# Kernel tuning notes

Hardware: AMD Instinct MI355X
Metric: run time of the kernel (lower is better)

The kernel has to match this reference:

```python
import jax, jax.numpy as jnp
import numpy as np

NUM_FREQ = 10
HIDDEN = 256
ENC_DIM = 2 * 2 * NUM_FREQ  # input_dim * 2 * num_frequencies = 40
OUT_DIM = 3


def setup_inputs() -> dict:
    key = jax.random.key(0)
    ks = jax.random.split(key, 8)
    B, N = 4, 262144
    x = jax.random.uniform(ks[0], (B, N, 2), dtype=jnp.float32)
    # layer 0: enc_dim -> hidden
    W_in = jax.random.normal(ks[1], (ENC_DIM, HIDDEN), dtype=jnp.float32) * (1.0 / np.sqrt(ENC_DIM))
    b_in = jnp.zeros((HIDDEN,), dtype=jnp.float32)
    # layers 1..6: hidden -> hidden (6 of them)
    W_hid = jax.random.normal(ks[2], (6, HIDDEN, HIDDEN), dtype=jnp.float32) * (1.0 / np.sqrt(HIDDEN))
    b_hid = jnp.zeros((6, HIDDEN), dtype=jnp.float32)
    # layer 7: hidden -> out
    W_out = jax.random.normal(ks[3], (HIDDEN, OUT_DIM), dtype=jnp.float32) * (1.0 / np.sqrt(HIDDEN))
    b_out = jnp.zeros((OUT_DIM,), dtype=jnp.float32)
    return {"x": x, "W_in": W_in, "b_in": b_in, "W_hid": W_hid,
            "b_hid": b_hid, "W_out": W_out, "b_out": b_out}


def _pos_encode(x):
    # x: (B, N, 2) -> (B, N, 40). Matches torch: cat([sin, cos], -1) over freq axis then flatten.
    freq = 2.0 ** jnp.arange(NUM_FREQ, dtype=jnp.float32)  # (10,)
    xe = x[..., :, None] * freq  # (B, N, 2, 10)
    enc = jnp.concatenate([jnp.sin(xe), jnp.cos(xe)], axis=-1)  # (B, N, 2, 20)
    return enc.reshape(x.shape[0], x.shape[1], -1)  # (B, N, 40)


def reference(x, W_in, b_in, W_hid, b_hid, W_out, b_out):
    h = _pos_encode(x)
    h = jax.nn.relu(h @ W_in + b_in)
    for i in range(W_hid.shape[0]):  # 6 hidden layers, fixed small loop
        h = jax.nn.relu(h @ W_hid[i] + b_hid[i])
    out = jnp.tanh(h @ W_out + b_out) / 100.0
    return out
```

## Files before the change

kernel.cpp:

```cpp
#include <hip/hip_runtime.h>
#include <stdint.h>

#define THREADS 256
#define NBLOCKS 8192
#define BR      128

#define NG_STRIDE 204800
#define WS_WOUT   819200
#define WS_TOTAL  (WS_WOUT + 16384)

typedef short bf16x8 __attribute__((ext_vector_type(8)));
typedef short bf16x4 __attribute__((ext_vector_type(4)));
typedef float f32x16 __attribute__((ext_vector_type(16)));
typedef float f32x4v __attribute__((ext_vector_type(4)));

__device__ __forceinline__ unsigned short f2bf(float f) {
    union { float f; unsigned int u; } v; v.f = f;
    unsigned int u = v.u;
    u += 0x7fffu + ((u >> 16) & 1u);
    return (unsigned short)(u >> 16);
}
__device__ __forceinline__ unsigned int cvt_pk_bf16(float lo, float hi) {
    unsigned int d;
    asm("v_cvt_pk_bf16_f32 %0, %1, %2" : "=v"(d) : "v"(lo), "v"(hi));
    return d;
}
__device__ __forceinline__ bf16x8 ld_act(const unsigned char* lo,
                                         const unsigned char* hi) {
    bf16x4 a = *(const bf16x4*)lo;
    bf16x4 b = *(const bf16x4*)hi;
    return __builtin_shufflevector(a, b, 0, 1, 2, 3, 4, 5, 6, 7);
}

__global__ void prep_kernel(const float* __restrict__ W_in,
                            const float* __restrict__ W_hid,
                            const float* __restrict__ W_out,
                            unsigned char* __restrict__ ws) {
    int id = blockIdx.x * 256 + threadIdx.x;
    if (id < 16384) {
        int n = id & 255, k = id >> 8;
        int ng = n >> 6, ft = (n >> 5) & 1, ln = n & 31;
        int kk = k >> 4, hi = (k >> 3) & 1, e = k & 7;
        float v = (k < 40) ? W_in[k * 256 + n] : 0.f;
        *(unsigned short*)(ws + ng * NG_STRIDE + (kk * 2 + ft) * 1024
                           + (hi * 32 + ln) * 16 + e * 2) = f2bf(v);
    } else if (id < 16384 + 393216) {
        int e2 = id - 16384;
        int l = e2 >> 16, r = e2 & 65535;
        int k = r >> 8, n = r & 255;
        int c = k >> 6, kk = (k >> 4) & 3, hi = (k >> 3) & 1, e = k & 7;
        int ng = n >> 6, ft = (n >> 5) & 1, ln = n & 31;
        float v = W_hid[l * 65536 + k * 256 + n];
        *(unsigned short*)(ws + ng * NG_STRIDE + 8192 + l * 32768
                           + ((c * 4 + kk) * 2 + ft) * 1024
                           + (hi * 32 + ln) * 16 + e * 2) = f2bf(v);
    } else if (id < 16384 + 393216 + 8192) {
        int e3 = id - 16384 - 393216;
        int n = e3 >> 8, k = e3 & 255;
        int kk = k >> 4, hi = (k >> 3) & 1, e = k & 7;
        float v = (n < 3) ? W_out[k * 3 + n] : 0.f;
        *(unsigned short*)(ws + WS_WOUT + kk * 1024
                           + (hi * 32 + n) * 16 + e * 2) = f2bf(v);
    }
}

template <int NC>
__device__ __forceinline__ void layer_pass(const unsigned char* __restrict__ wl,
                                           const float* __restrict__ bp,
                                           unsigned char* actL, f32x16 (&acc)[2][4],
                                           int nblk, int l31,
                                           int hi, int hi16,
                                           int rswz, int rswz2) {
    #pragma unroll
    for (int tn = 0; tn < 2; ++tn) {
        #pragma unroll
        for (int g4 = 0; g4 < 4; ++g4) {
            f32x4v bv = *(const f32x4v*)(bp + nblk + tn * 32 + g4 * 8 + hi * 4);
            #pragma unroll
            for (int tr = 0; tr < 4; ++tr) {
                #pragma unroll
                for (int j = 0; j < 4; ++j)
                    acc[tn][tr][g4 * 4 + j] = bv[j];
            }
        }
    }

    const unsigned char* base = actL + l31 * 512;

    __builtin_amdgcn_s_setprio(1);
    #pragma unroll
    for (int c = 0; c < NC; ++c) {
        #pragma unroll
        for (int kk = 0; kk < 4; ++kk) {
            const unsigned char* fp = wl + (c * 4 + kk) * 2048;
            bf16x8 a0 = *(const bf16x8*)(fp);
            bf16x8 a1 = *(const bf16x8*)(fp + 1024);
            const int bo  = c * 128 + kk * 32 + hi16;
            const int olo = bo ^ rswz;
            const int ohi = bo ^ rswz2;
            bf16x8 b0 = ld_act(base +           olo, base +           ohi);
            bf16x8 b1 = ld_act(base + 16384   + olo, base + 16384   + ohi);
            bf16x8 b2 = ld_act(base + 32768   + olo, base + 32768   + ohi);
            bf16x8 b3 = ld_act(base + 49152   + olo, base + 49152   + ohi);
            acc[0][0] = __builtin_amdgcn_mfma_f32_32x32x16_bf16(a0, b0, acc[0][0], 0, 0, 0);
            acc[1][0] = __builtin_amdgcn_mfma_f32_32x32x16_bf16(a1, b0, acc[1][0], 0, 0, 0);
            acc[0][1] = __builtin_amdgcn_mfma_f32_32x32x16_bf16(a0, b1, acc[0][1], 0, 0, 0);
            acc[1][1] = __builtin_amdgcn_mfma_f32_32x32x16_bf16(a1, b1, acc[1][1], 0, 0, 0);
            acc[0][2] = __builtin_amdgcn_mfma_f32_32x32x16_bf16(a0, b2, acc[0][2], 0, 0, 0);
            acc[1][2] = __builtin_amdgcn_mfma_f32_32x32x16_bf16(a1, b2, acc[1][2], 0, 0, 0);
            acc[0][3] = __builtin_amdgcn_mfma_f32_32x32x16_bf16(a0, b3, acc[0][3], 0, 0, 0);
            acc[1][3] = __builtin_amdgcn_mfma_f32_32x32x16_bf16(a1, b3, acc[1][3], 0, 0, 0);
        }
    }
    __builtin_amdgcn_s_setprio(0);

    __syncthreads();
    #pragma unroll
    for (int tr = 0; tr < 4; ++tr) {
        unsigned char* rowp = actL + (tr * 32 + l31) * 512;
        #pragma unroll
        for (int tn = 0; tn < 2; ++tn) {
            #pragma unroll
            for (int g4 = 0; g4 < 4; ++g4) {
                float v0 = fmaxf(acc[tn][tr][g4 * 4 + 0], 0.f);
                float v1 = fmaxf(acc[tn][tr][g4 * 4 + 1], 0.f);
                float v2 = fmaxf(acc[tn][tr][g4 * 4 + 2], 0.f);
                float v3 = fmaxf(acc[tn][tr][g4 * 4 + 3], 0.f);
                int n0b = (nblk + tn * 32 + g4 * 8 + hi * 4) * 2;
                uint2 u; u.x = cvt_pk_bf16(v0, v1); u.y = cvt_pk_bf16(v2, v3);
                *(uint2*)(rowp + (n0b ^ rswz)) = u;
            }
        }
    }
    __syncthreads();
}

__global__ __launch_bounds__(THREADS, 2)
void nerf_main(const float* __restrict__ x,
               const float* __restrict__ b_in,
               const float* __restrict__ b_hid,
               const float* __restrict__ b_out,
               const unsigned char* __restrict__ ws,
               float* __restrict__ out) {
    __shared__ __align__(16) unsigned char actL[65536];

    const int tid  = threadIdx.x;
    const int lane = tid & 63;
    const int wv   = tid >> 6;
    const int l31  = lane & 31;
    const int hi   = lane >> 5;
    const int hi16 = hi << 4;
    const int rswz  = (l31 & 15) << 3;
    const int rswz2 = rswz ^ 8;
    const int nblk = wv * 64;
    const long gr0 = (long)blockIdx.x * BR;

    #pragma unroll
    for (int pass = 0; pass < 2; ++pass) {
        const int rr = (tid >> 2) + pass * 64;
        const int part = tid & 3;
        const int co = part >> 1, hf = part & 1;
        float xv = x[(gr0 + rr) * 2 + co];
        unsigned char* rowp = actL + rr * 512;
        const int rsw = (rr & 15) << 3;
        const int kb = co * 20 + hf * 10;
        float vv[10];
        #pragma unroll
        for (int f = 0; f < 10; ++f) {
            float ang = xv * (float)(1 << f);
            vv[f] = hf ? __cosf(ang) : __sinf(ang);
        }
        #pragma unroll
        for (int p = 0; p < 5; ++p) {
            unsigned int u = cvt_pk_bf16(vv[2 * p], vv[2 * p + 1]);
            int byte = (kb + 2 * p) * 2;
            *(unsigned int*)(rowp + (byte ^ rsw)) = u;
        }
        int z = 80 + part * 12;
        *(unsigned int*)(rowp + ((z    ) ^ rsw)) = 0u;
        *(unsigned int*)(rowp + ((z + 4) ^ rsw)) = 0u;
        *(unsigned int*)(rowp + ((z + 8) ^ rsw)) = 0u;
    }
    __syncthreads();

    f32x16 acc[2][4];
    const unsigned char* wstream = ws + wv * NG_STRIDE + lane * 16;

    layer_pass<1>(wstream, b_in, actL, acc, nblk, l31, hi, hi16, rswz, rswz2);
    wstream += 8192;

    #pragma unroll 1
    for (int l = 0; l < 6; ++l) {
        layer_pass<4>(wstream, b_hid + l * 256,
                      actL, acc, nblk, l31, hi, hi16, rswz, rswz2);
        wstream += 32768;
    }

    {
        f32x16 c0, c1;
        #pragma unroll
        for (int j = 0; j < 16; ++j) { c0[j] = 0.f; c1[j] = 0.f; }
        const unsigned char* wo   = ws + WS_WOUT + lane * 16;
        const unsigned char* arow = actL + (wv * 32 + l31) * 512;
        #pragma unroll
        for (int kk = 0; kk < 16; ++kk) {
            bf16x8 a = *(const bf16x8*)(wo + kk * 1024);
            const int bo = kk * 32 + hi16;
            bf16x8 b = ld_act(arow + (bo ^ rswz), arow + (bo ^ rswz2));
            if (kk & 1) c1 = __builtin_amdgcn_mfma_f32_32x32x16_bf16(a, b, c1, 0, 0, 0);
            else        c0 = __builtin_amdgcn_mfma_f32_32x32x16_bf16(a, b, c0, 0, 0, 0);
        }
        if (hi == 0) {
            long row = gr0 + wv * 32 + l31;
            float* op = out + row * 3;
            #pragma unroll
            for (int j = 0; j < 3; ++j)
                op[j] = tanhf(c0[j] + c1[j] + b_out[j]) * 0.01f;
        }
    }
}

extern "C" void kernel_launch(void* const* d_in, const int* in_sizes, int n_in,
                              void* d_out, int out_size, void* d_ws, size_t ws_size,
                              hipStream_t stream) {
    (void)in_sizes; (void)n_in; (void)out_size;
    const float* x     = (const float*)d_in[0];
    const float* W_in  = (const float*)d_in[1];
    const float* b_in  = (const float*)d_in[2];
    const float* W_hid = (const float*)d_in[3];
    const float* b_hid = (const float*)d_in[4];
    const float* W_out = (const float*)d_in[5];
    const float* b_out = (const float*)d_in[6];
    unsigned char* ws  = (unsigned char*)d_ws;
    float* out = (float*)d_out;

    if (ws_size < (size_t)WS_TOTAL) return;

    prep_kernel<<<1632, 256, 0, stream>>>(W_in, W_hid, W_out, ws);
    nerf_main<<<NBLOCKS, THREADS, 0, stream>>>(x, b_in, b_hid, b_out, ws, out);
}
```

Measured before the change: 726.1 us.

## Shrink row tile to 96 to fit three blocks per CU

Reduces rows per block from 128 to 96, cutting the LDS activation buffer to 48KB and the accumulator array to 2x3 tiles so three blocks can be resident per CU (launch bounds raised to 3). Activation LDS addresses are precomputed once per kernel as pointer arrays and no longer rebuilt inside each layer. The grid is now derived from the input size, with bounds checks for the tail block. The cost is less weight reuse per block, since each weight fragment now feeds 3 MFMAs instead of 4, which raises weight load traffic per row, and one wave sits idle in the final output layer.

```diff
diff --git a/kernel.cpp b/kernel.cpp
--- a/kernel.cpp
+++ b/kernel.cpp
@@ -2,8 +2,7 @@
 #include <stdint.h>
 
 #define THREADS 256
-#define NBLOCKS 8192
-#define BR      128
+#define BR      96
 
 #define NG_STRIDE 204800
 #define WS_WOUT   819200
@@ -67,25 +66,24 @@
 template <int NC>
 __device__ __forceinline__ void layer_pass(const unsigned char* __restrict__ wl,
                                            const float* __restrict__ bp,
-                                           unsigned char* actL, f32x16 (&acc)[2][4],
+                                           unsigned char* actL, f32x16 (&acc)[2][3],
+                                           const unsigned char* const (&alo)[4],
+                                           const unsigned char* const (&ahi)[4],
                                            int nblk, int l31,
-                                           int hi, int hi16,
-                                           int rswz, int rswz2) {
+                                           int hi, int rswz) {
     #pragma unroll
     for (int tn = 0; tn < 2; ++tn) {
         #pragma unroll
         for (int g4 = 0; g4 < 4; ++g4) {
             f32x4v bv = *(const f32x4v*)(bp + nblk + tn * 32 + g4 * 8 + hi * 4);
             #pragma unroll
-            for (int tr = 0; tr < 4; ++tr) {
+            for (int tr = 0; tr < 3; ++tr) {
                 #pragma unroll
                 for (int j = 0; j < 4; ++j)
                     acc[tn][tr][g4 * 4 + j] = bv[j];
             }
         }
     }
-
-    const unsigned char* base = actL + l31 * 512;
 
     __builtin_amdgcn_s_setprio(1);
     #pragma unroll
@@ -95,28 +93,23 @@
             const unsigned char* fp = wl + (c * 4 + kk) * 2048;
             bf16x8 a0 = *(const bf16x8*)(fp);
             bf16x8 a1 = *(const bf16x8*)(fp + 1024);
-            const int bo  = c * 128 + kk * 32 + hi16;
-            const int olo = bo ^ rswz;
-            const int ohi = bo ^ rswz2;
-            bf16x8 b0 = ld_act(base +           olo, base +           ohi);
-            bf16x8 b1 = ld_act(base + 16384   + olo, base + 16384   + ohi);
-            bf16x8 b2 = ld_act(base + 32768   + olo, base + 32768   + ohi);
-            bf16x8 b3 = ld_act(base + 49152   + olo, base + 49152   + ohi);
+            const int cb = c * 128;
+            bf16x8 b0 = ld_act(alo[kk] + cb,          ahi[kk] + cb);
+            bf16x8 b1 = ld_act(alo[kk] + 16384 + cb,  ahi[kk] + 16384 + cb);
+            bf16x8 b2 = ld_act(alo[kk] + 32768 + cb,  ahi[kk] + 32768 + cb);
             acc[0][0] = __builtin_amdgcn_mfma_f32_32x32x16_bf16(a0, b0, acc[0][0], 0, 0, 0);
             acc[1][0] = __builtin_amdgcn_mfma_f32_32x32x16_bf16(a1, b0, acc[1][0], 0, 0, 0);
             acc[0][1] = __builtin_amdgcn_mfma_f32_32x32x16_bf16(a0, b1, acc[0][1], 0, 0, 0);
             acc[1][1] = __builtin_amdgcn_mfma_f32_32x32x16_bf16(a1, b1, acc[1][1], 0, 0, 0);
             acc[0][2] = __builtin_amdgcn_mfma_f32_32x32x16_bf16(a0, b2, acc[0][2], 0, 0, 0);
             acc[1][2] = __builtin_amdgcn_mfma_f32_32x32x16_bf16(a1, b2, acc[1][2], 0, 0, 0);
-            acc[0][3] = __builtin_amdgcn_mfma_f32_32x32x16_bf16(a0, b3, acc[0][3], 0, 0, 0);
-            acc[1][3] = __builtin_amdgcn_mfma_f32_32x32x16_bf16(a1, b3, acc[1][3], 0, 0, 0);
         }
     }
     __builtin_amdgcn_s_setprio(0);
 
     __syncthreads();
     #pragma unroll
-    for (int tr = 0; tr < 4; ++tr) {
+    for (int tr = 0; tr < 3; ++tr) {
         unsigned char* rowp = actL + (tr * 32 + l31) * 512;
         #pragma unroll
         for (int tn = 0; tn < 2; ++tn) {
@@ -135,14 +128,14 @@
     __syncthreads();
 }
 
-__global__ __launch_bounds__(THREADS, 2)
+__global__ __launch_bounds__(THREADS, 3)
 void nerf_main(const float* __restrict__ x,
                const float* __restrict__ b_in,
                const float* __restrict__ b_hid,
                const float* __restrict__ b_out,
                const unsigned char* __restrict__ ws,
-               float* __restrict__ out) {
-    __shared__ __align__(16) unsigned char actL[65536];
+               float* __restrict__ out, long ntot) {
+    __shared__ __align__(16) unsigned char actL[49152];
 
     const int tid  = threadIdx.x;
     const int lane = tid & 63;
@@ -158,45 +151,57 @@
     #pragma unroll
     for (int pass = 0; pass < 2; ++pass) {
         const int rr = (tid >> 2) + pass * 64;
-        const int part = tid & 3;
-        const int co = part >> 1, hf = part & 1;
-        float xv = x[(gr0 + rr) * 2 + co];
-        unsigned char* rowp = actL + rr * 512;
-        const int rsw = (rr & 15) << 3;
-        const int kb = co * 20 + hf * 10;
-        float vv[10];
-        #pragma unroll
-        for (int f = 0; f < 10; ++f) {
-            float ang = xv * (float)(1 << f);
-            vv[f] = hf ? __cosf(ang) : __sinf(ang);
-        }
-        #pragma unroll
-        for (int p = 0; p < 5; ++p) {
-            unsigned int u = cvt_pk_bf16(vv[2 * p], vv[2 * p + 1]);
-            int byte = (kb + 2 * p) * 2;
-            *(unsigned int*)(rowp + (byte ^ rsw)) = u;
-        }
-        int z = 80 + part * 12;
-        *(unsigned int*)(rowp + ((z    ) ^ rsw)) = 0u;
-        *(unsigned int*)(rowp + ((z + 4) ^ rsw)) = 0u;
-        *(unsigned int*)(rowp + ((z + 8) ^ rsw)) = 0u;
+        if (rr < BR) {
+            const int part = tid & 3;
+            const int co = part >> 1, hf = part & 1;
+            const long grow = gr0 + rr;
+            float xv = (grow < ntot) ? x[grow * 2 + co] : 0.f;
+            unsigned char* rowp = actL + rr * 512;
+            const int rsw = (rr & 15) << 3;
+            const int kb = co * 20 + hf * 10;
+            float vv[10];
+            #pragma unroll
+            for (int f = 0; f < 10; ++f) {
+                float ang = xv * (float)(1 << f);
+                vv[f] = hf ? __cosf(ang) : __sinf(ang);
+            }
+            #pragma unroll
+            for (int p = 0; p < 5; ++p) {
+                unsigned int u = cvt_pk_bf16(vv[2 * p], vv[2 * p + 1]);
+                int byte = (kb + 2 * p) * 2;
+                *(unsigned int*)(rowp + (byte ^ rsw)) = u;
+            }
+            int z = 80 + part * 12;
+            *(unsigned int*)(rowp + ((z    ) ^ rsw)) = 0u;
+            *(unsigned int*)(rowp + ((z + 4) ^ rsw)) = 0u;
+            *(unsigned int*)(rowp + ((z + 8) ^ rsw)) = 0u;
+        }
     }
     __syncthreads();
 
-    f32x16 acc[2][4];
+    const unsigned char* alo[4];
+    const unsigned char* ahi[4];
+    #pragma unroll
+    for (int kk = 0; kk < 4; ++kk) {
+        const int bo = kk * 32 + hi16;
+        alo[kk] = actL + l31 * 512 + (bo ^ rswz);
+        ahi[kk] = actL + l31 * 512 + (bo ^ rswz2);
+    }
+
+    f32x16 acc[2][3];
     const unsigned char* wstream = ws + wv * NG_STRIDE + lane * 16;
 
-    layer_pass<1>(wstream, b_in, actL, acc, nblk, l31, hi, hi16, rswz, rswz2);
+    layer_pass<1>(wstream, b_in, actL, acc, alo, ahi, nblk, l31, hi, rswz);
     wstream += 8192;
 
     #pragma unroll 1
     for (int l = 0; l < 6; ++l) {
         layer_pass<4>(wstream, b_hid + l * 256,
-                      actL, acc, nblk, l31, hi, hi16, rswz, rswz2);
+                      actL, acc, alo, ahi, nblk, l31, hi, rswz);
         wstream += 32768;
     }
 
-    {
+    if (wv < 3) {
         f32x16 c0, c1;
         #pragma unroll
         for (int j = 0; j < 16; ++j) { c0[j] = 0.f; c1[j] = 0.f; }
@@ -212,10 +217,12 @@
         }
         if (hi == 0) {
             long row = gr0 + wv * 32 + l31;
-            float* op = out + row * 3;
-            #pragma unroll
-            for (int j = 0; j < 3; ++j)
-                op[j] = tanhf(c0[j] + c1[j] + b_out[j]) * 0.01f;
+            if (row < ntot) {
+                float* op = out + row * 3;
+                #pragma unroll
+                for (int j = 0; j < 3; ++j)
+                    op[j] = tanhf(c0[j] + c1[j] + b_out[j]) * 0.01f;
+            }
         }
     }
 }
@@ -223,7 +230,7 @@
 extern "C" void kernel_launch(void* const* d_in, const int* in_sizes, int n_in,
                               void* d_out, int out_size, void* d_ws, size_t ws_size,
                               hipStream_t stream) {
-    (void)in_sizes; (void)n_in; (void)out_size;
+    (void)n_in; (void)out_size;
     const float* x     = (const float*)d_in[0];
     const float* W_in  = (const float*)d_in[1];
     const float* b_in  = (const float*)d_in[2];
@@ -236,6 +243,9 @@
 
     if (ws_size < (size_t)WS_TOTAL) return;
 
+    const long ntot = (long)in_sizes[0] / 2;
+    const int  grid = (int)((ntot + BR - 1) / BR);
+
     prep_kernel<<<1632, 256, 0, stream>>>(W_in, W_hid, W_out, ws);
-    nerf_main<<<NBLOCKS, THREADS, 0, stream>>>(x, b_in, b_hid, b_out, ws, out);
-}
+    nerf_main<<<grid, THREADS, 0, stream>>>(x, b_in, b_hid, b_out, ws, out, ntot);
+}
```

After: 2.129 ms. +193.2%, slower.
